# Performance work log

Measured on AMD Instinct MI355X. Metric: run time of the kernel, lower is better.

## Reference

```python
import jax, jax.numpy as jnp
import numpy as np

N_NODES = 100000
N_EDGES = 3200000
N_GRAPHS = 64


def setup_inputs() -> dict:
    key = jax.random.key(0)
    ks = jax.random.split(key, 16)
    s = 0.1
    pos = jax.random.normal(ks[0], (N_NODES, 2), dtype=jnp.float32) * 100.0
    w1a = jax.random.normal(ks[1], (4, 32), dtype=jnp.float32) * s
    b1a = jax.random.normal(ks[2], (32,), dtype=jnp.float32) * s
    w1b = jax.random.normal(ks[3], (32, 32), dtype=jnp.float32) * s
    b1b = jax.random.normal(ks[4], (32,), dtype=jnp.float32) * s
    w2a = jax.random.normal(ks[5], (34, 32), dtype=jnp.float32) * s
    b2a = jax.random.normal(ks[6], (32,), dtype=jnp.float32) * s
    w2b = jax.random.normal(ks[7], (32, 32), dtype=jnp.float32) * s
    b2b = jax.random.normal(ks[8], (32,), dtype=jnp.float32) * s
    wc = jax.random.normal(ks[9], (32, 3), dtype=jnp.float32) * s
    bc = jax.random.normal(ks[10], (3,), dtype=jnp.float32) * s
    edge_index = jax.random.randint(ks[11], (2, N_EDGES), 0, N_NODES, dtype=jnp.int64)
    batch = jnp.sort(jax.random.randint(ks[12], (N_NODES,), 0, N_GRAPHS, dtype=jnp.int64))
    return {"pos": pos, "w1a": w1a, "b1a": b1a, "w1b": w1b, "b1b": b1b,
            "w2a": w2a, "b2a": b2a, "w2b": w2b, "b2b": b2b,
            "wc": wc, "bc": bc, "edge_index": edge_index, "batch": batch}


def _seg_max0(x, seg, n):
    # segment max with empty segments filled with 0 (PyG scatter-max semantics)
    m = jax.ops.segment_max(x, seg, num_segments=n)
    return jnp.where(jnp.isfinite(m), m, 0.0)


def _pointnet_layer(h, pos, src, dst, w1, b1, w2, b2):
    # message: mlp(cat[h_j, pos_j - pos_i]); aggr: max over incoming edges at i
    x = jnp.concatenate([h[src], pos[src] - pos[dst]], axis=-1)  # [E, C+2]
    m = jnp.maximum(x @ w1 + b1, 0.0) @ w2 + b2                   # [E, 32]
    return _seg_max0(m, dst, N_NODES)                             # [N, 32]


def reference(pos, w1a, b1a, w1b, b1b, w2a, b2a, w2b, b2b, wc, bc,
              edge_index, batch):
    src, dst = edge_index[0], edge_index[1]  # messages flow src(j) -> dst(i)
    h = jax.nn.relu(_pointnet_layer(pos, pos, src, dst, w1a, b1a, w1b, b1b))
    h = jax.nn.relu(_pointnet_layer(h, pos, src, dst, w2a, b2a, w2b, b2b))
    g = _seg_max0(h, batch, N_GRAPHS)        # global max pool per graph
    return g @ wc + bc                        # [G, 3]
```

## Files before the change

kernel.cpp:

```cpp
#include <hip/hip_runtime.h>
#include <hip/hip_bf16.h>


#define NEG_BIG (-3.0e38f)
#define BSHIFT 9
#define NBMAX 256
#define CHUNKC 4096
#define CHUNKS 16384

typedef __attribute__((ext_vector_type(8))) short short8;
typedef __attribute__((ext_vector_type(4))) float f32x4;
typedef __attribute__((ext_vector_type(4))) unsigned uint4v;

__device__ __forceinline__ short bf16r(float f) {
    unsigned u = __float_as_uint(f);
    unsigned r = (u + 0x7FFFu + ((u >> 16) & 1u)) >> 16;
    return (short)r;
}
__device__ __forceinline__ unsigned pack_bf16(float lo, float hi) {
    return ((unsigned)(unsigned short)bf16r(lo)) |
           (((unsigned)(unsigned short)bf16r(hi)) << 16);
}

__global__ __launch_bounds__(256) void wprep_kernel(
    const float* __restrict__ w1b, const float* __restrict__ w2b,
    unsigned* __restrict__ wfbuf)
{
    int t = threadIdx.x;
    int l = t >> 7, frag = (t >> 6) & 1, lane = t & 63;
    const float* w = l ? w2b : w1b;
    int m16 = lane & 15, kq = (lane >> 4) * 8;
    int cb = frag * 16 + m16;
    unsigned out[4];
#pragma unroll
    for (int p = 0; p < 4; ++p)
        out[p] = pack_bf16(w[(kq + 2 * p) * 32 + cb], w[(kq + 2 * p + 1) * 32 + cb]);
    *(uint4v*)(wfbuf + (size_t)t * 4) = (uint4v){out[0], out[1], out[2], out[3]};
}

__global__ __launch_bounds__(256) void pre1_kernel(
    const float* __restrict__ pos, const float* __restrict__ w1a,
    const float* __restrict__ b1a, unsigned* __restrict__ Abf,
    unsigned* __restrict__ Bbf, int N)
{
    int t = blockIdx.x * 256 + threadIdx.x;
    if (t >= N * 16) return;
    int n = t >> 4, c0 = (t & 15) * 2;
    float px = pos[2 * n], py = pos[2 * n + 1];
    float a[2], b[2];
#pragma unroll
    for (int i = 0; i < 2; ++i) {
        int c = c0 + i;
        float w0 = w1a[c], w1 = w1a[32 + c], w2 = w1a[64 + c], w3 = w1a[96 + c];
        a[i] = fmaf(px, w0 + w2, fmaf(py, w1 + w3, b1a[c]));
        b[i] = -(px * w2 + py * w3);
    }
    Abf[t] = pack_bf16(a[0], a[1]);
    Bbf[t] = pack_bf16(b[0], b[1]);
}

__global__ __launch_bounds__(256) void pre2_kernel(
    const float* __restrict__ pos, const float* __restrict__ h1,
    const float* __restrict__ w2a, const float* __restrict__ b2a,
    unsigned* __restrict__ Abf, unsigned* __restrict__ Bbf, int N)
{
    int n = blockIdx.x * 256 + threadIdx.x;
    if (n >= N) return;
    float px = pos[2 * n], py = pos[2 * n + 1];
    const float4* hq = (const float4*)(h1 + (size_t)n * 32);
    float4 hv[8];
#pragma unroll
    for (int q = 0; q < 8; ++q) hv[q] = hq[q];
    float acc[32];
#pragma unroll
    for (int c = 0; c < 32; ++c)
        acc[c] = fmaf(px, w2a[1024 + c], fmaf(py, w2a[1056 + c], b2a[c]));
    const float* hf = (const float*)hv;
#pragma unroll
    for (int k = 0; k < 32; ++k) {
        float hk = hf[k];
#pragma unroll
        for (int c = 0; c < 32; ++c) acc[c] = fmaf(hk, w2a[k * 32 + c], acc[c]);
    }
    unsigned* Arow = Abf + (size_t)n * 16;
    unsigned* Brow = Bbf + (size_t)n * 16;
#pragma unroll
    for (int p = 0; p < 16; ++p) {
        Arow[p] = pack_bf16(acc[2 * p], acc[2 * p + 1]);
        Brow[p] = pack_bf16(-(px * w2a[1024 + 2 * p] + py * w2a[1056 + 2 * p]),
                            -(px * w2a[1025 + 2 * p] + py * w2a[1057 + 2 * p]));
    }
}

__global__ __launch_bounds__(256) void bucket_count_kernel(
    const int* __restrict__ ei, int* __restrict__ btot, int E, int NB)
{
    __shared__ int bh[NBMAX];
    int tid = threadIdx.x;
    for (int i = tid; i < NB; i += 256) bh[i] = 0;
    __syncthreads();
    const int* dsts = ei + E;
    int base0 = blockIdx.x * CHUNKC;
    for (int i = tid * 4; i < CHUNKC; i += 1024) {
        int e = base0 + i;
        if (e + 3 < E) {
            int4 d = *(const int4*)(dsts + e);
            atomicAdd(&bh[d.x >> BSHIFT], 1);
            atomicAdd(&bh[d.y >> BSHIFT], 1);
            atomicAdd(&bh[d.z >> BSHIFT], 1);
            atomicAdd(&bh[d.w >> BSHIFT], 1);
        } else {
            for (int k = e; k < E && k < e + 4; ++k)
                atomicAdd(&bh[dsts[k] >> BSHIFT], 1);
        }
    }
    __syncthreads();
    for (int i = tid; i < NB; i += 256)
        if (bh[i]) atomicAdd(btot + i, bh[i]);
}

__global__ __launch_bounds__(256) void scan_bucket_kernel(
    const int* __restrict__ tot, int* __restrict__ base_,
    int* __restrict__ cur_, int NB)
{
    __shared__ int ws_[4], wo[4];
    int tid = threadIdx.x, lane = tid & 63, wv = tid >> 6;
    int v = (tid < NB) ? tot[tid] : 0;
    int x = v;
#pragma unroll
    for (int d = 1; d < 64; d <<= 1) {
        int t = __shfl_up(x, d, 64);
        if (lane >= d) x += t;
    }
    if (lane == 63) ws_[wv] = x;
    __syncthreads();
    if (tid == 0) { int r = 0; for (int w = 0; w < 4; ++w) { wo[w] = r; r += ws_[w]; } }
    __syncthreads();
    int ex = wo[wv] + x - v;
    if (tid < NB) { base_[tid] = ex; cur_[tid] = ex; }
}

__global__ __launch_bounds__(256) void bucket_scatter_kernel(
    const int* __restrict__ ei, int* __restrict__ bcur,
    int* __restrict__ csr_tmp, int E, int NB)
{
    __shared__ int lh[NBMAX];
    __shared__ int lb[NBMAX];
    int tid = threadIdx.x;
    for (int i = tid; i < NB; i += 256) lh[i] = 0;
    __syncthreads();
    const int* dsts = ei + E;
    int base0 = blockIdx.x * CHUNKS;
    for (int i = tid * 4; i < CHUNKS; i += 1024) {
        int e = base0 + i;
        if (e + 3 < E) {
            int4 d = *(const int4*)(dsts + e);
            atomicAdd(&lh[d.x >> BSHIFT], 1);
            atomicAdd(&lh[d.y >> BSHIFT], 1);
            atomicAdd(&lh[d.z >> BSHIFT], 1);
            atomicAdd(&lh[d.w >> BSHIFT], 1);
        } else {
            for (int k = e; k < E && k < e + 4; ++k)
                atomicAdd(&lh[dsts[k] >> BSHIFT], 1);
        }
    }
    __syncthreads();
    for (int i = tid; i < NB; i += 256) {
        int c = lh[i];
        lb[i] = c ? atomicAdd(bcur + i, c) : 0;
    }
    __syncthreads();
    for (int i = tid; i < NB; i += 256) lh[i] = 0;
    __syncthreads();
    for (int i = tid * 4; i < CHUNKS; i += 1024) {
        int e = base0 + i;
        if (e + 3 < E) {
            int4 s = *(const int4*)(ei + e);
            int4 d = *(const int4*)(dsts + e);
            int b, o;
            b = d.x >> BSHIFT; o = atomicAdd(&lh[b], 1);
            csr_tmp[lb[b] + o] = s.x | ((d.x & 511) << 20);
            b = d.y >> BSHIFT; o = atomicAdd(&lh[b], 1);
            csr_tmp[lb[b] + o] = s.y | ((d.y & 511) << 20);
            b = d.z >> BSHIFT; o = atomicAdd(&lh[b], 1);
            csr_tmp[lb[b] + o] = s.z | ((d.z & 511) << 20);
            b = d.w >> BSHIFT; o = atomicAdd(&lh[b], 1);
            csr_tmp[lb[b] + o] = s.w | ((d.w & 511) << 20);
        } else {
            for (int k = e; k < E && k < e + 4; ++k) {
                int dd = dsts[k];
                int b = dd >> BSHIFT;
                int o = atomicAdd(&lh[b], 1);
                csr_tmp[lb[b] + o] = ei[k] | ((dd & 511) << 20);
            }
        }
    }
}

__global__ __launch_bounds__(256) void place_kernel(
    const int* __restrict__ csr_tmp, const int* __restrict__ bbase,
    const int* __restrict__ bcur, int* __restrict__ pcur,
    int* __restrict__ csr_src, int* __restrict__ tile_dst, int N)
{
    __shared__ int cnt[128], pre[128], cur[128];
    __shared__ int pstart_s;
    int fb = blockIdx.x, tid = threadIdx.x;
    int cb = fb >> 2, qq = fb & 3;
    int d0 = fb << 7;
    int start = bbase[cb], end = bcur[cb];
    if (tid < 128) cnt[tid] = 0;
    __syncthreads();
    for (int i = start + tid; i < end; i += 256) {
        int rec = csr_tmp[i];
        if (((rec >> 27) & 3) == qq) atomicAdd(&cnt[(rec >> 20) & 127], 1);
    }
    __syncthreads();
    if (tid < 64) {
        int lane = tid;
        int a0 = (cnt[2 * lane] + 15) & ~15;
        int a1 = (cnt[2 * lane + 1] + 15) & ~15;
        int s = a0 + a1;
        int x = s;
#pragma unroll
        for (int d = 1; d < 64; d <<= 1) {
            int t = __shfl_up(x, d, 64);
            if (lane >= d) x += t;
        }
        int total = __shfl(x, 63, 64);
        if (lane == 0) pstart_s = total ? atomicAdd(pcur, total) : 0;
        int ex = x - s;
        pre[2 * lane] = ex;      pre[2 * lane + 1] = ex + a0;
        cur[2 * lane] = ex;      cur[2 * lane + 1] = ex + a0;
    }
    __syncthreads();
    int pstart = pstart_s;
    for (int i = start + tid; i < end; i += 256) {
        int rec = csr_tmp[i];
        if (((rec >> 27) & 3) == qq) {
            int p = atomicAdd(&cur[(rec >> 20) & 127], 1);
            csr_src[pstart + p] = rec & 0xFFFFF;
        }
    }
    if (tid < 128) {
        int d = d0 + tid;
        if (d < N) {
            int c = cnt[tid], pc = (c + 15) & ~15;
            int base = pstart + pre[tid];
            for (int k = c; k < pc; ++k) csr_src[base + k] = -1;
            int tb = base >> 4, nt = pc >> 4;
            for (int k = 0; k < nt; ++k) tile_dst[tb + k] = d;
        }
    }
}

__global__ __launch_bounds__(256, 4) void edge_layer_kernel(
    const int* __restrict__ csr_src, const int* __restrict__ tile_dst,
    const unsigned* __restrict__ Abf, const unsigned* __restrict__ Bbf,
    const unsigned* __restrict__ wf, const float* __restrict__ bias,
    unsigned int* __restrict__ hout)
{
    int tid = threadIdx.x;
    int lane = tid & 63;
    int wv = tid >> 6;
    int wbase = blockIdx.x * 256 + wv * 64;
    int m16 = lane & 15;
    int q = lane >> 4;
    int kq = q * 8;
    int ch = (lane < 16) ? m16 : (16 + m16);

    int td[4];
#pragma unroll
    for (int eg = 0; eg < 4; ++eg) td[eg] = tile_dst[(wbase >> 4) + eg];
    if (td[0] < 0 && td[1] < 0 && td[2] < 0 && td[3] < 0) return;

    short8 bf0 = __builtin_bit_cast(short8, *(const uint4v*)(wf + (size_t)lane * 4));
    short8 bf1 = __builtin_bit_cast(short8, *(const uint4v*)(wf + (size_t)(64 + lane) * 4));
    float myb = bias[ch];

    int src[4];
#pragma unroll
    for (int eg = 0; eg < 4; ++eg) {
        int sidx = wbase + eg * 16 + m16;
        src[eg] = (td[eg] >= 0) ? csr_src[sidx] : -1;
    }

    uint4v ua4[4], ub4[4];
#pragma unroll
    for (int eg = 0; eg < 4; ++eg) {
        int brow = (td[eg] >= 0) ? td[eg] : 0;
        int arow = (src[eg] >= 0) ? src[eg] : brow;
        ua4[eg] = *(const uint4v*)(Abf + (size_t)arow * 16 + (kq >> 1));
        ub4[eg] = *(const uint4v*)(Bbf + (size_t)brow * 16 + (kq >> 1));
    }

    f32x4 zero = {0.0f, 0.0f, 0.0f, 0.0f};
    float cv0 = NEG_BIG, cv1 = NEG_BIG;
    int cdst = -1;
#pragma unroll
    for (int eg = 0; eg < 4; ++eg) {
        unsigned long long bal = __ballot(src[eg] >= 0);
        uint4v pk;
#pragma unroll
        for (int d = 0; d < 4; ++d) {
            unsigned uad = ua4[eg][d], ubd = ub4[eg][d];
            float a0 = __uint_as_float(uad << 16);
            float a1 = __uint_as_float(uad & 0xFFFF0000u);
            float b0 = __uint_as_float(ubd << 16);
            float b1 = __uint_as_float(ubd & 0xFFFF0000u);
            float r0 = fmaxf(a0 + b0, 0.0f);
            float r1 = fmaxf(a1 + b1, 0.0f);
            pk[d] = __builtin_amdgcn_perm(__float_as_uint(r1),
                                          __float_as_uint(r0), 0x07060302u);
        }
        short8 af = __builtin_bit_cast(short8, pk);
        f32x4 d0 = __builtin_amdgcn_mfma_f32_16x16x32_bf16(af, bf0, zero, 0, 0, 0);
        f32x4 d1 = __builtin_amdgcn_mfma_f32_16x16x32_bf16(af, bf1, zero, 0, 0, 0);
        float v0, v1;
        if (bal == ~0ull) {
            v0 = fmaxf(fmaxf(d0[0], d0[1]), fmaxf(d0[2], d0[3]));
            v1 = fmaxf(fmaxf(d1[0], d1[1]), fmaxf(d1[2], d1[3]));
        } else {
            v0 = NEG_BIG; v1 = NEG_BIG;
#pragma unroll
            for (int r = 0; r < 4; ++r) {
                bool ok = (bal >> (q * 4 + r)) & 1ull;
                v0 = fmaxf(v0, ok ? d0[r] : NEG_BIG);
                v1 = fmaxf(v1, ok ? d1[r] : NEG_BIG);
            }
        }
        v0 = fmaxf(v0, __shfl_xor(v0, 16, 64));
        v0 = fmaxf(v0, __shfl_xor(v0, 32, 64));
        v1 = fmaxf(v1, __shfl_xor(v1, 16, 64));
        v1 = fmaxf(v1, __shfl_xor(v1, 32, 64));
        int d = td[eg];
        if (d != cdst) {
            if (cdst >= 0 && lane < 32) {
                float x = ((lane < 16) ? cv0 : cv1) + myb;
                if (x > 0.0f)
                    atomicMax(hout + (size_t)cdst * 32 + ch, __float_as_uint(x));
            }
            cdst = d; cv0 = v0; cv1 = v1;
        } else {
            cv0 = fmaxf(cv0, v0); cv1 = fmaxf(cv1, v1);
        }
    }
    if (cdst >= 0 && lane < 32) {
        float x = ((lane < 16) ? cv0 : cv1) + myb;
        if (x > 0.0f)
            atomicMax(hout + (size_t)cdst * 32 + ch, __float_as_uint(x));
    }
}

__global__ __launch_bounds__(256) void pool_kernel(
    const float* __restrict__ h2, const int* __restrict__ batch,
    unsigned int* __restrict__ gbuf, int N)
{
    int g = blockIdx.x, p = blockIdx.y;
    __shared__ int sbound[2];
    __shared__ float red[256];
    if (threadIdx.x < 2) {
        int target = g + (int)threadIdx.x;
        int lo = 0, hi = N;
        while (lo < hi) {
            int mid = (lo + hi) >> 1;
            if (batch[mid] < target) lo = mid + 1; else hi = mid;
        }
        sbound[threadIdx.x] = lo;
    }
    __syncthreads();
    int start = sbound[0], end = sbound[1];
    int c = threadIdx.x & 31, r = threadIdx.x >> 5;
    float mx = 0.0f;
    for (int n = start + p * 8 + r; n < end; n += 128)
        mx = fmaxf(mx, h2[(size_t)n * 32 + c]);
    red[threadIdx.x] = mx;
    __syncthreads();
    if (r < 4) red[threadIdx.x] = fmaxf(red[threadIdx.x], red[threadIdx.x + 128]);
    __syncthreads();
    if (r < 2) red[threadIdx.x] = fmaxf(red[threadIdx.x], red[threadIdx.x + 64]);
    __syncthreads();
    if (r == 0) {
        float v = fmaxf(red[threadIdx.x], red[threadIdx.x + 32]);
        if (v > 0.0f) atomicMax(gbuf + g * 32 + c, __float_as_uint(v));
    }
}

__global__ __launch_bounds__(192) void out_kernel(
    const float* __restrict__ gbuf, const float* __restrict__ wc,
    const float* __restrict__ bc, float* __restrict__ out, int G)
{
    int t = threadIdx.x;
    if (t >= G * 3) return;
    int g = t / 3, j = t % 3;
    float s = bc[j];
#pragma unroll
    for (int c = 0; c < 32; ++c)
        s = fmaf(gbuf[g * 32 + c], wc[c * 3 + j], s);
    out[t] = s;
}

extern "C" void kernel_launch(void* const* d_in, const int* in_sizes, int n_in,
                              void* d_out, int out_size, void* d_ws, size_t ws_size,
                              hipStream_t stream) {
    const float* pos = (const float*)d_in[0];
    const float* w1a = (const float*)d_in[1];
    const float* b1a = (const float*)d_in[2];
    const float* w1b = (const float*)d_in[3];
    const float* b1b = (const float*)d_in[4];
    const float* w2a = (const float*)d_in[5];
    const float* b2a = (const float*)d_in[6];
    const float* w2b = (const float*)d_in[7];
    const float* b2b = (const float*)d_in[8];
    const float* wc  = (const float*)d_in[9];
    const float* bc  = (const float*)d_in[10];
    const int* ei    = (const int*)d_in[11];
    const int* batch = (const int*)d_in[12];

    const int N = in_sizes[12];
    const int E = in_sizes[11] / 2;
    const int G = out_size / 3;
    const size_t NC = (size_t)N * 32;
    const int NB = (N + 511) >> BSHIFT;
    const int NF = NB * 4;
    const int SMAX = (E + 15 * ((N < E) ? N : E) + 255) & ~255;
    const int TMAX = SMAX >> 4;

    int* btot    = (int*)d_ws;
    int* pcur    = btot + 256;
    int* bbase   = pcur + 256;
    int* bcur    = bbase + 256;
    unsigned* wfbuf = (unsigned*)(bcur + 256);
    int* csr_src = (int*)(wfbuf + 1024);
    int* tile_dst = csr_src + SMAX;
    unsigned* Abf = (unsigned*)(tile_dst + TMAX);
    unsigned* Bbf = Abf + (size_t)N * 16;
    float* h1    = (float*)(Bbf + (size_t)N * 16);
    float* h2    = h1 + NC;
    float* gbuf  = h2 + NC;
    int* csr_tmp = (int*)Abf;

    int npBlocks = ((int)(N * 16) + 255) / 256;
    int nBlocks  = (N + 255) / 256;
    int cBlocks  = (E + CHUNKC - 1) / CHUNKC;
    int sBlocks  = (E + CHUNKS - 1) / CHUNKS;
    int edBlocks = (SMAX + 255) / 256;

    hipMemsetAsync(btot, 0, 512 * sizeof(int), stream);
    hipMemsetAsync(gbuf, 0, (size_t)G * 32 * sizeof(float), stream);
    hipMemsetAsync(tile_dst, 0xFF, (size_t)TMAX * sizeof(int), stream);
    hipMemsetAsync(h1, 0, 2 * NC * sizeof(float), stream);

    wprep_kernel<<<1, 256, 0, stream>>>(w1b, w2b, wfbuf);
    bucket_count_kernel<<<cBlocks, 256, 0, stream>>>(ei, btot, E, NB);
    scan_bucket_kernel<<<1, 256, 0, stream>>>(btot, bbase, bcur, NB);
    bucket_scatter_kernel<<<sBlocks, 256, 0, stream>>>(ei, bcur, csr_tmp, E, NB);
    place_kernel<<<NF, 256, 0, stream>>>(csr_tmp, bbase, bcur, pcur,
                                         csr_src, tile_dst, N);

    pre1_kernel<<<npBlocks, 256, 0, stream>>>(pos, w1a, b1a, Abf, Bbf, N);
    edge_layer_kernel<<<edBlocks, 256, 0, stream>>>(csr_src, tile_dst, Abf, Bbf,
                                                    wfbuf, b1b, (unsigned int*)h1);
    pre2_kernel<<<nBlocks, 256, 0, stream>>>(pos, h1, w2a, b2a, Abf, Bbf, N);
    edge_layer_kernel<<<edBlocks, 256, 0, stream>>>(csr_src, tile_dst, Abf, Bbf,
                                                    wfbuf + 512, b2b,
                                                    (unsigned int*)h2);
    pool_kernel<<<dim3(G, 16), 256, 0, stream>>>(h2, batch,
                                                 (unsigned int*)gbuf, N);
    out_kernel<<<1, 192, 0, stream>>>(gbuf, wc, bc, (float*)d_out, G);
}
```

Before: 342.9 us.

## Place one bucket per 1024-thread block and cache bucket records in LDS

The placement kernel now handles a whole 512-node bucket per block with 1024 threads, instead of four 256-thread blocks that each scanned the full bucket and filtered by quarter. Records are cached in a 64KB shared array during the counting pass so the second pass rereads them from LDS. This removes the 4x redundant global reads of csr_tmp and one of the two read passes. In exchange there are fewer, larger blocks (about 196) with heavy LDS use, which limits occupancy. Buckets larger than the cache fall back to global reads.

```diff
diff --git a/kernel.cpp b/kernel.cpp
--- a/kernel.cpp
+++ b/kernel.cpp
@@ -7,6 +7,7 @@
 #define NBMAX 256
 #define CHUNKC 4096
 #define CHUNKS 16384
+#define RCAP 16384
 
 typedef __attribute__((ext_vector_type(8))) short short8;
 typedef __attribute__((ext_vector_type(4))) float f32x4;
@@ -197,29 +198,35 @@
     }
 }
 
-__global__ __launch_bounds__(256) void place_kernel(
+__global__ __launch_bounds__(1024) void place_kernel(
     const int* __restrict__ csr_tmp, const int* __restrict__ bbase,
     const int* __restrict__ bcur, int* __restrict__ pcur,
     int* __restrict__ csr_src, int* __restrict__ tile_dst, int N)
 {
-    __shared__ int cnt[128], pre[128], cur[128];
+    __shared__ int rec_cache[RCAP];
+    __shared__ int cnt[512], pre[512], cur[512];
     __shared__ int pstart_s;
-    int fb = blockIdx.x, tid = threadIdx.x;
-    int cb = fb >> 2, qq = fb & 3;
-    int d0 = fb << 7;
-    int start = bbase[cb], end = bcur[cb];
-    if (tid < 128) cnt[tid] = 0;
-    __syncthreads();
-    for (int i = start + tid; i < end; i += 256) {
-        int rec = csr_tmp[i];
-        if (((rec >> 27) & 3) == qq) atomicAdd(&cnt[(rec >> 20) & 127], 1);
+    int b = blockIdx.x, tid = threadIdx.x;
+    int d0 = b << BSHIFT;
+    int start = bbase[b], end = bcur[b];
+    int len = end - start;
+    if (tid < 512) cnt[tid] = 0;
+    __syncthreads();
+    for (int i = tid; i < len; i += 1024) {
+        int rec = csr_tmp[start + i];
+        if (i < RCAP) rec_cache[i] = rec;
+        atomicAdd(&cnt[rec >> 20], 1);
     }
     __syncthreads();
     if (tid < 64) {
         int lane = tid;
-        int a0 = (cnt[2 * lane] + 15) & ~15;
-        int a1 = (cnt[2 * lane + 1] + 15) & ~15;
-        int s = a0 + a1;
+        int a[8];
+        int s = 0;
+#pragma unroll
+        for (int j = 0; j < 8; ++j) {
+            a[j] = (cnt[8 * lane + j] + 15) & ~15;
+            s += a[j];
+        }
         int x = s;
 #pragma unroll
         for (int d = 1; d < 64; d <<= 1) {
@@ -228,20 +235,22 @@
         }
         int total = __shfl(x, 63, 64);
         if (lane == 0) pstart_s = total ? atomicAdd(pcur, total) : 0;
-        int ex = x - s;
-        pre[2 * lane] = ex;      pre[2 * lane + 1] = ex + a0;
-        cur[2 * lane] = ex;      cur[2 * lane + 1] = ex + a0;
+        int run = x - s;
+#pragma unroll
+        for (int j = 0; j < 8; ++j) {
+            pre[8 * lane + j] = run;
+            cur[8 * lane + j] = run;
+            run += a[j];
+        }
     }
     __syncthreads();
     int pstart = pstart_s;
-    for (int i = start + tid; i < end; i += 256) {
-        int rec = csr_tmp[i];
-        if (((rec >> 27) & 3) == qq) {
-            int p = atomicAdd(&cur[(rec >> 20) & 127], 1);
-            csr_src[pstart + p] = rec & 0xFFFFF;
-        }
-    }
-    if (tid < 128) {
+    for (int i = tid; i < len; i += 1024) {
+        int rec = (i < RCAP) ? rec_cache[i] : csr_tmp[start + i];
+        int p = atomicAdd(&cur[rec >> 20], 1);
+        csr_src[pstart + p] = rec & 0xFFFFF;
+    }
+    if (tid < 512) {
         int d = d0 + tid;
         if (d < N) {
             int c = cnt[tid], pc = (c + 15) & ~15;
@@ -421,7 +430,6 @@
     const int G = out_size / 3;
     const size_t NC = (size_t)N * 32;
     const int NB = (N + 511) >> BSHIFT;
-    const int NF = NB * 4;
     const int SMAX = (E + 15 * ((N < E) ? N : E) + 255) & ~255;
     const int TMAX = SMAX >> 4;
 
@@ -454,8 +462,8 @@
     bucket_count_kernel<<<cBlocks, 256, 0, stream>>>(ei, btot, E, NB);
     scan_bucket_kernel<<<1, 256, 0, stream>>>(btot, bbase, bcur, NB);
     bucket_scatter_kernel<<<sBlocks, 256, 0, stream>>>(ei, bcur, csr_tmp, E, NB);
-    place_kernel<<<NF, 256, 0, stream>>>(csr_tmp, bbase, bcur, pcur,
-                                         csr_src, tile_dst, N);
+    place_kernel<<<NB, 1024, 0, stream>>>(csr_tmp, bbase, bcur, pcur,
+                                          csr_src, tile_dst, N);
 
     pre1_kernel<<<npBlocks, 256, 0, stream>>>(pos, w1a, b1a, Abf, Bbf, N);
     edge_layer_kernel<<<edBlocks, 256, 0, stream>>>(csr_src, tile_dst, Abf, Bbf,
```

After: 314.2 us. 1.09x faster.
